# Kernel tuning notes

Measured on AMD Instinct MI355X. Metric: run time of the kernel, lower is better.

Reference implementation:

```python
import jax, jax.numpy as jnp
import numpy as np

B, T, C, H, W = 16, 32, 64, 16, 16
NUM_FEAT = 10


def setup_inputs() -> dict:
    key = jax.random.key(0)
    ks = jax.random.split(key, 8)
    CHW = C * H * W
    G = NUM_FEAT * H * W
    init = lambda k, shape, fan: jax.random.normal(k, shape, jnp.float32) / np.sqrt(fan).astype(np.float32)
    return {
        "input": jax.random.normal(ks[0], (B, T, C, H, W), jnp.float32),
        "input1": jax.random.normal(ks[1], (B, T, C, H, W), jnp.float32),  # unused by forward
        "act_weights": jax.random.uniform(ks[2], (3,), jnp.float32),
        "conv1_w": init(ks[3], (NUM_FEAT, CHW), CHW),   # Conv1d kernel_size=1 -> plain matmul weight
        "conv1_b": jnp.zeros((NUM_FEAT,), jnp.float32),
        "G3_w": init(ks[4], (G, CHW), CHW),
        "G3_b": jnp.zeros((G,), jnp.float32),
        "ffnn1_w": init(ks[5], (T, T), T),              # torch Linear weight [out,in]
        "ffnn1_b": jnp.zeros((T,), jnp.float32),
    }


def reference(input, input1, act_weights, conv1_w, conv1_b, G3_w, G3_b, ffnn1_w, ffnn1_b):
    Bb, Tt, Cc, Hh, Ww = input.shape
    x = input.reshape(Bb, Tt, Cc * Hh * Ww)                       # [B,T,CHW] (== transposed conv1d input)
    # conv1 (1x1 conv) -> [B,T,F]; AvgPool1d(num_feat) over feature dim -> [B,T]
    f = jnp.einsum('btc,fc->btf', x, conv1_w) + conv1_b
    pooled = f.mean(axis=-1)                                      # [B,T]
    # ffnn1: Linear(T,T): y = pooled @ W^T + b
    z = jnp.einsum('bt,st->bs', pooled, ffnn1_w) + ffnn1_b        # [B,T]
    # G3 (1x1 conv) -> [B,T,G] with G = num_feat*H*W (original permutes to [B,T,G])
    g = jnp.einsum('btc,gc->btg', x, G3_w) + G3_b
    # diag_embed(act(z)) @ g is exactly a per-(b,t) elementwise scale of g.
    gates = (act_weights[0] * jax.nn.relu(z)
             + act_weights[1] * jax.nn.sigmoid(z)
             + act_weights[2] * jax.nn.softmax(z, axis=1))        # softmax over T (dim=1)
    out = (gates[:, :, None] * g).reshape(Bb, Tt, NUM_FEAT, Hh, Ww)
    return out
```

## Files before the change

kernel.cpp:

```cpp
#include <hip/hip_runtime.h>
#include <hip/hip_bf16.h>

#define K_DIM 16384
#define M_DIM 512
#define N_DIM 2560
#define BM 256
#define BN 160
#define BK 64
#define KSPLIT 8
#define KCH (K_DIM / KSPLIT)
#define NT (KCH / BK)

typedef float f32x4 __attribute__((ext_vector_type(4)));
typedef __bf16 bf16x8 __attribute__((ext_vector_type(8)));

__device__ __forceinline__ unsigned short f2bf(float f){
  union { float f; unsigned u; } v; v.f = f;
  unsigned r = v.u + 0x7FFFu + ((v.u >> 16) & 1u);
  return (unsigned short)(r >> 16);
}
__device__ __forceinline__ unsigned bfpack2(float lo, float hi){
  return (unsigned)f2bf(lo) | ((unsigned)f2bf(hi) << 16);
}
__device__ __forceinline__ unsigned cpk2(float lo, float hi){
  __bf16 a = (__bf16)lo, b = (__bf16)hi;
  unsigned short ua = __builtin_bit_cast(unsigned short, a);
  unsigned short ub = __builtin_bit_cast(unsigned short, b);
  return (unsigned)ua | ((unsigned)ub << 16);
}
__device__ __forceinline__ unsigned short cbf(float f){
  __bf16 a = (__bf16)f;
  return __builtin_bit_cast(unsigned short, a);
}

__global__ __launch_bounds__(256)
void prep_kernel(const float* __restrict__ conv1_w, const float* __restrict__ conv1_b,
                 float* __restrict__ w_mean, float* __restrict__ b_mean)
{
  int c = blockIdx.x * 256 + threadIdx.x;
  if (c < K_DIM){
    float s = 0.f;
    #pragma unroll
    for (int f = 0; f < 10; ++f) s += conv1_w[f * K_DIM + c];
    w_mean[c] = s * 0.1f;
  }
  if (blockIdx.x == 0 && threadIdx.x == 0){
    float s = 0.f;
    #pragma unroll
    for (int f = 0; f < 10; ++f) s += conv1_b[f];
    *b_mean = s * 0.1f;
  }
}

__global__ __launch_bounds__(256)
void pooled_kernel(const float* __restrict__ X, const float* __restrict__ w_mean,
                   const float* __restrict__ b_mean, float* __restrict__ pooled,
                   unsigned short* __restrict__ xbf)
{
  const int row = blockIdx.x;
  const int tid = threadIdx.x;
  const float* xr = X + (size_t)row * K_DIM;
  unsigned short* xb = xbf + (size_t)row * K_DIM;
  float s = 0.f;
  #pragma unroll 2
  for (int i = 0; i < 8; ++i){
    int idx = (tid + 256 * i) * 8;
    float4 a0 = *(const float4*)(xr + idx);
    float4 a1 = *(const float4*)(xr + idx + 4);
    float4 w0 = *(const float4*)(w_mean + idx);
    float4 w1 = *(const float4*)(w_mean + idx + 4);
    s += a0.x*w0.x + a0.y*w0.y + a0.z*w0.z + a0.w*w0.w
       + a1.x*w1.x + a1.y*w1.y + a1.z*w1.z + a1.w*w1.w;
    uint4 p;
    p.x = bfpack2(a0.x, a0.y); p.y = bfpack2(a0.z, a0.w);
    p.z = bfpack2(a1.x, a1.y); p.w = bfpack2(a1.z, a1.w);
    *(uint4*)(xb + idx) = p;
  }
  #pragma unroll
  for (int off = 32; off; off >>= 1) s += __shfl_down(s, off);
  __shared__ float red[4];
  if ((tid & 63) == 0) red[tid >> 6] = s;
  __syncthreads();
  if (tid == 0) pooled[row] = red[0] + red[1] + red[2] + red[3] + *b_mean;
}

__global__ __launch_bounds__(512)
void gates_kernel(const float* __restrict__ pooled, const float* __restrict__ fw,
                  const float* __restrict__ fb, const float* __restrict__ aw,
                  float* __restrict__ gates)
{
  __shared__ float ps[512];
  int tid = threadIdx.x;
  ps[tid] = pooled[tid];
  __syncthreads();
  int b = tid >> 5, s = tid & 31;
  float z = fb[s];
  #pragma unroll
  for (int t = 0; t < 32; ++t) z += ps[b * 32 + t] * fw[s * 32 + t];
  float mx = z;
  #pragma unroll
  for (int off = 16; off; off >>= 1) mx = fmaxf(mx, __shfl_xor(mx, off));
  float e = expf(z - mx);
  float sum = e;
  #pragma unroll
  for (int off = 16; off; off >>= 1) sum += __shfl_xor(sum, off);
  float sm = e / sum;
  float relu = z > 0.f ? z : 0.f;
  float sig = 1.f / (1.f + expf(-z));
  gates[tid] = aw[0] * relu + aw[1] * sig + aw[2] * sm;
}

__global__ __launch_bounds__(512, 2)
void gemm_kernel(const unsigned short* __restrict__ Abf, const float* __restrict__ W,
                 void* __restrict__ outp, int mode)
{
  __shared__ __align__(16) char smem[106496];

  const int tid  = threadIdx.x;
  const int lane = tid & 63;
  const int wv   = tid >> 6;
  const int wm   = (wv >> 1) * 64;
  const int wn   = (wv & 1) * 80;

  const int id = blockIdx.x;
  const int kz = id & 7;
  const int r  = id >> 3;
  const int m0 = (r & 1) * BM;
  const int n0 = (r >> 1) * BN;
  const int kbase = kz * KCH;

  f32x4 acc[4][5] = {};

  const int arow0 = tid >> 3;
  const int ac8   = (tid & 7) ^ (arow0 & 7);
  const unsigned short* asrc = Abf + (size_t)(m0 + arow0) * K_DIM + ac8 * 8;
  const int adst = tid * 16;

  auto stageA = [&](int abuf, int k0){
    char* dst = smem + (abuf << 15);
    #pragma unroll
    for (int j = 0; j < 4; ++j){
      __builtin_amdgcn_global_load_lds(
        (const __attribute__((address_space(1))) void*)(asrc + (size_t)j * 64 * K_DIM + k0),
        (__attribute__((address_space(3))) void*)(dst + j * 8192 + adst),
        16, 0, 0);
    }
  };

  const float* bsrcs[5];
  int boff[5];
  #pragma unroll
  for (int j = 0; j < 5; ++j){
    int u = j * 512 + tid;
    int brow = u >> 4;
    int bc4  = u & 15;
    bsrcs[j] = W + (size_t)(n0 + brow) * K_DIM + kbase + bc4 * 4;
    boff[j]  = brow * 128 + ((bc4 * 8) ^ ((brow & 7) << 4));
  }

  float4 rb[5];
  auto loadB = [&](int kt){
    #pragma unroll
    for (int j = 0; j < 5; ++j) rb[j] = *(const float4*)(bsrcs[j] + kt * BK);
  };
  auto writeB = [&](int bbuf){
    char* dst = smem + 65536 + bbuf * 20480;
    #pragma unroll
    for (int j = 0; j < 5; ++j){
      uint2 u;
      u.x = cpk2(rb[j].x, rb[j].y);
      u.y = cpk2(rb[j].z, rb[j].w);
      *(uint2*)(dst + boff[j]) = u;
    }
  };

  auto compute = [&](int abuf, int bbuf){
    const char* A_ = smem + (abuf << 15);
    const char* B_ = smem + 65536 + bbuf * 20480;
    #pragma unroll
    for (int kk = 0; kk < 2; ++kk){
      bf16x8 af[4], bfv[5];
      const int kbyte = kk * 64 + (lane >> 4) * 16;
      #pragma unroll
      for (int i = 0; i < 4; ++i){
        int row = wm + i * 16 + (lane & 15);
        af[i] = *(const bf16x8*)(A_ + row * 128 + (kbyte ^ ((row & 7) << 4)));
      }
      #pragma unroll
      for (int j = 0; j < 5; ++j){
        int rowb = wn + j * 16 + (lane & 15);
        bfv[j] = *(const bf16x8*)(B_ + rowb * 128 + (kbyte ^ ((rowb & 7) << 4)));
      }
      __builtin_amdgcn_s_setprio(1);
      #pragma unroll
      for (int i = 0; i < 4; ++i)
        #pragma unroll
        for (int j = 0; j < 5; ++j)
          acc[i][j] = __builtin_amdgcn_mfma_f32_16x16x32_bf16(af[i], bfv[j], acc[i][j], 0, 0, 0);
      __builtin_amdgcn_s_setprio(0);
    }
  };

  loadB(0);
  stageA(0, kbase);
  writeB(0);
  loadB(1);
  stageA(1, kbase + BK);
  asm volatile("s_waitcnt vmcnt(9) lgkmcnt(0)" ::: "memory");
  __builtin_amdgcn_s_barrier();
  __builtin_amdgcn_sched_barrier(0);

  for (int t = 0; t < NT; ++t){
    writeB((t + 1) & 1);
    loadB(t + 2 < NT ? t + 2 : NT - 1);
    compute(t & 1, t & 1);
    asm volatile("s_waitcnt vmcnt(5) lgkmcnt(0)" ::: "memory");
    __builtin_amdgcn_s_barrier();
    __builtin_amdgcn_sched_barrier(0);
    if (t + 2 < NT)
      stageA(t & 1, kbase + (t + 2) * BK);
  }

  if (mode == 0){
    unsigned short* P = (unsigned short*)outp + (size_t)kz * M_DIM * N_DIM;
    #pragma unroll
    for (int i = 0; i < 4; ++i){
      int rbase = m0 + wm + i * 16 + (lane >> 4) * 4;
      #pragma unroll
      for (int j = 0; j < 5; ++j){
        int col = n0 + wn + j * 16 + (lane & 15);
        #pragma unroll
        for (int r2 = 0; r2 < 4; ++r2)
          P[(size_t)(rbase + r2) * N_DIM + col] = cbf(acc[i][j][r2]);
      }
    }
  } else {
    float* P = (float*)outp;
    #pragma unroll
    for (int i = 0; i < 4; ++i){
      int rbase = m0 + wm + i * 16 + (lane >> 4) * 4;
      #pragma unroll
      for (int j = 0; j < 5; ++j){
        int col = n0 + wn + j * 16 + (lane & 15);
        #pragma unroll
        for (int r2 = 0; r2 < 4; ++r2)
          atomicAdd(&P[(size_t)(rbase + r2) * N_DIM + col], acc[i][j][r2]);
      }
    }
  }
}

__global__ __launch_bounds__(256)
void reduce_kernel(const unsigned short* __restrict__ part, const float* __restrict__ gates,
                   const float* __restrict__ bias, float* __restrict__ out, int ksplit)
{
  int i8 = blockIdx.x * 256 + threadIdx.x;
  if (i8 >= M_DIM * N_DIM / 8) return;
  size_t off = (size_t)i8 * 8;
  int m = (int)(off / N_DIM);
  int n = (int)(off % N_DIM);
  float s[8] = {};
  for (int z = 0; z < ksplit; ++z){
    uint4 p = *(const uint4*)(part + (size_t)z * M_DIM * N_DIM + off);
    unsigned w[4] = { p.x, p.y, p.z, p.w };
    #pragma unroll
    for (int q = 0; q < 4; ++q){
      union { unsigned u; float f; } lo, hi;
      lo.u = (w[q] & 0xFFFFu) << 16;
      hi.u = (w[q] & 0xFFFF0000u);
      s[2*q]   += lo.f;
      s[2*q+1] += hi.f;
    }
  }
  float g = gates[m];
  float4 b0 = *(const float4*)(bias + n);
  float4 b1 = *(const float4*)(bias + n + 4);
  float4 o0, o1;
  o0.x = g * (s[0] + b0.x); o0.y = g * (s[1] + b0.y);
  o0.z = g * (s[2] + b0.z); o0.w = g * (s[3] + b0.w);
  o1.x = g * (s[4] + b1.x); o1.y = g * (s[5] + b1.y);
  o1.z = g * (s[6] + b1.z); o1.w = g * (s[7] + b1.w);
  *(float4*)(out + off) = o0;
  *(float4*)(out + off + 4) = o1;
}

__global__ __launch_bounds__(256)
void finalize_kernel(float* __restrict__ out, const float* __restrict__ gates,
                     const float* __restrict__ bias)
{
  int i4 = blockIdx.x * 256 + threadIdx.x;
  if (i4 >= M_DIM * N_DIM / 4) return;
  size_t off = (size_t)i4 * 4;
  int m = (int)(off / N_DIM);
  int n = (int)(off % N_DIM);
  float4 o = *(const float4*)(out + off);
  float4 bv = *(const float4*)(bias + n);
  float g = gates[m];
  o.x = g * (o.x + bv.x); o.y = g * (o.y + bv.y);
  o.z = g * (o.z + bv.z); o.w = g * (o.w + bv.w);
  *(float4*)(out + off) = o;
}

extern "C" void kernel_launch(void* const* d_in, const int* in_sizes, int n_in,
                              void* d_out, int out_size, void* d_ws, size_t ws_size,
                              hipStream_t stream)
{
  const float* input   = (const float*)d_in[0];
  const float* aw      = (const float*)d_in[2];
  const float* conv1_w = (const float*)d_in[3];
  const float* conv1_b = (const float*)d_in[4];
  const float* G3_w    = (const float*)d_in[5];
  const float* G3_b    = (const float*)d_in[6];
  const float* ffnn1_w = (const float*)d_in[7];
  const float* ffnn1_b = (const float*)d_in[8];
  float* out = (float*)d_out;

  float* wsf    = (float*)d_ws;
  float* w_mean = wsf;
  float* pooled = wsf + 16384;
  float* gates  = wsf + 16896;
  float* b_mean = wsf + 17408;
  unsigned short* xbf = (unsigned short*)(wsf + 17472);
  unsigned short* partial = xbf + (size_t)M_DIM * K_DIM;

  const size_t need_det = (size_t)17472 * 4 + (size_t)M_DIM * K_DIM * 2
                          + (size_t)KSPLIT * M_DIM * N_DIM * 2;

  prep_kernel<<<64, 256, 0, stream>>>(conv1_w, conv1_b, w_mean, b_mean);
  pooled_kernel<<<512, 256, 0, stream>>>(input, w_mean, b_mean, pooled, xbf);
  gates_kernel<<<1, 512, 0, stream>>>(pooled, ffnn1_w, ffnn1_b, aw, gates);

  const int grid = (M_DIM / BM) * (N_DIM / BN) * KSPLIT;
  if (ws_size >= need_det){
    gemm_kernel<<<grid, 512, 0, stream>>>(xbf, G3_w, partial, 0);
    const int n8 = M_DIM * N_DIM / 8;
    reduce_kernel<<<(n8 + 255) / 256, 256, 0, stream>>>(partial, gates, G3_b, out, KSPLIT);
  } else {
    (void)hipMemsetAsync(d_out, 0, (size_t)out_size * sizeof(float), stream);
    gemm_kernel<<<grid, 512, 0, stream>>>(xbf, G3_w, d_out, 2);
    const int n4 = M_DIM * N_DIM / 4;
    finalize_kernel<<<(n4 + 255) / 256, 256, 0, stream>>>(out, gates, G3_b);
  }
}
```

Measured before the change: 83.74 us.

## Deepen GEMM pipeline to triple-buffered A and double register B prefetch

The GEMM main loop moves from a two-stage to a three-stage pipeline. A tiles are triple-buffered in LDS, with shared memory growing from 104KB to 136KB. B tiles are prefetched three iterations ahead using two alternating register sets. The goal is to hide more global-memory latency behind MFMA compute, at the cost of more LDS and VGPR pressure, which may reduce occupancy below the declared two blocks per CU.

After: 89.81 us. +7.2%, slower.

```diff
diff --git a/kernel.cpp b/kernel.cpp
--- a/kernel.cpp
+++ b/kernel.cpp
@@ -114,7 +114,7 @@
 void gemm_kernel(const unsigned short* __restrict__ Abf, const float* __restrict__ W,
                  void* __restrict__ outp, int mode)
 {
-  __shared__ __align__(16) char smem[106496];
+  __shared__ __align__(16) char smem[139264];
 
   const int tid  = threadIdx.x;
   const int lane = tid & 63;
@@ -137,7 +137,7 @@
   const int adst = tid * 16;
 
   auto stageA = [&](int abuf, int k0){
-    char* dst = smem + (abuf << 15);
+    char* dst = smem + abuf * 32768;
     #pragma unroll
     for (int j = 0; j < 4; ++j){
       __builtin_amdgcn_global_load_lds(
@@ -158,25 +158,24 @@
     boff[j]  = brow * 128 + ((bc4 * 8) ^ ((brow & 7) << 4));
   }
 
-  float4 rb[5];
-  auto loadB = [&](int kt){
-    #pragma unroll
-    for (int j = 0; j < 5; ++j) rb[j] = *(const float4*)(bsrcs[j] + kt * BK);
+  auto loadB = [&](int kt, float4* rr){
+    #pragma unroll
+    for (int j = 0; j < 5; ++j) rr[j] = *(const float4*)(bsrcs[j] + kt * BK);
   };
-  auto writeB = [&](int bbuf){
-    char* dst = smem + 65536 + bbuf * 20480;
+  auto writeB = [&](int bbuf, const float4* rr){
+    char* dst = smem + 98304 + bbuf * 20480;
     #pragma unroll
     for (int j = 0; j < 5; ++j){
       uint2 u;
-      u.x = cpk2(rb[j].x, rb[j].y);
-      u.y = cpk2(rb[j].z, rb[j].w);
+      u.x = cpk2(rr[j].x, rr[j].y);
+      u.y = cpk2(rr[j].z, rr[j].w);
       *(uint2*)(dst + boff[j]) = u;
     }
   };
 
   auto compute = [&](int abuf, int bbuf){
-    const char* A_ = smem + (abuf << 15);
-    const char* B_ = smem + 65536 + bbuf * 20480;
+    const char* A_ = smem + abuf * 32768;
+    const char* B_ = smem + 98304 + bbuf * 20480;
     #pragma unroll
     for (int kk = 0; kk < 2; ++kk){
       bf16x8 af[4], bfv[5];
@@ -201,25 +200,37 @@
     }
   };
 
-  loadB(0);
+  float4 rbA[5], rbB[5];
+
+  loadB(0, rbA);
   stageA(0, kbase);
-  writeB(0);
-  loadB(1);
+  writeB(0, rbA);
+  loadB(1, rbA);
+  loadB(2, rbB);
   stageA(1, kbase + BK);
-  asm volatile("s_waitcnt vmcnt(9) lgkmcnt(0)" ::: "memory");
+  asm volatile("s_waitcnt vmcnt(14) lgkmcnt(0)" ::: "memory");
   __builtin_amdgcn_s_barrier();
   __builtin_amdgcn_sched_barrier(0);
-
-  for (int t = 0; t < NT; ++t){
-    writeB((t + 1) & 1);
-    loadB(t + 2 < NT ? t + 2 : NT - 1);
-    compute(t & 1, t & 1);
-    asm volatile("s_waitcnt vmcnt(5) lgkmcnt(0)" ::: "memory");
-    __builtin_amdgcn_s_barrier();
-    __builtin_amdgcn_sched_barrier(0);
-    if (t + 2 < NT)
-      stageA(t & 1, kbase + (t + 2) * BK);
-  }
+  stageA(2, kbase + 2 * BK);
+
+  int aCur = 0;
+  #define STEP(T, RCUR, RNEXT)                                           \
+    do {                                                                 \
+      if ((T) + 1 < NT) writeB(((T) + 1) & 1, RCUR);   \
+      loadB((T) + 3 < NT ? (T) + 3 : NT - 1, RCUR);    \
+      compute(aCur, (T) & 1);                                            \
+      asm volatile("s_waitcnt vmcnt(14) lgkmcnt(0)" ::: "memory");       \
+      __builtin_amdgcn_s_barrier();                                      \
+      __builtin_amdgcn_sched_barrier(0);                                 \
+      if ((T) + 3 < NT) stageA(aCur, kbase + ((T) + 3) * BK);            \
+      aCur = (aCur == 2) ? 0 : aCur + 1;                                 \
+    } while (0)
+
+  for (int t = 0; t < NT; t += 2){
+    STEP(t, rbA, rbB);
+    STEP(t + 1, rbB, rbA);
+  }
+  #undef STEP
 
   if (mode == 0){
     unsigned short* P = (unsigned short*)outp + (size_t)kz * M_DIM * N_DIM;
```
